# Optimization experiments

Hardware: AMD Instinct MI355X
Metric: run time of the kernel (lower is better)

The kernel has to match this reference:

```python
import jax, jax.numpy as jnp
import numpy as np

B, NPER, K = 32, 256, 32
N, E = B * NPER, B * NPER * 32
H, NF, NG, L = 128, 128, 50, 6
CUTOFF = 10.0
LOG2 = 0.6931471805599453


def _ssp(x):
    # ShiftedSoftplus: softplus(x) - log(2)
    return jax.nn.softplus(x) - LOG2


def setup_inputs() -> dict:
    key = jax.random.key(0)
    ks = jax.random.split(key, 16)
    rng = np.random.default_rng(0)

    pos = jnp.asarray(rng.uniform(0.0, 5.0, size=(N, 3)).astype(np.float32))
    z = jnp.asarray(rng.integers(1, 100, size=(N,)).astype(np.int32))
    batch = jnp.asarray((np.arange(N) // NPER).astype(np.int32))
    # K neighbors per atom, within the same graph, no self-loops; dst sorted
    dst = np.repeat(np.arange(N), K)
    off = rng.integers(1, NPER, size=N * K)
    src = (dst % NPER + off) % NPER + (dst // NPER) * NPER
    edge_index = jnp.asarray(np.stack([src, dst]).astype(np.int32))
    domain_ids = jnp.asarray(rng.integers(0, 5, size=(B,)).astype(np.int32))

    def dense(k, i, o):
        return jax.random.normal(k, (i, o), jnp.float32) / np.sqrt(i)

    def stackw(k, i, o):
        return jax.random.normal(k, (L, i, o), jnp.float32) / np.sqrt(i)

    return {
        'pos': pos, 'z': z, 'batch': batch, 'edge_index': edge_index,
        'domain_ids': domain_ids,
        'embedding': jax.random.normal(ks[0], (100, H), jnp.float32),
        'mlp_w1': stackw(ks[1], NG, NF), 'mlp_b1': jnp.zeros((L, NF), jnp.float32),
        'mlp_w2': stackw(ks[2], NF, NF), 'mlp_b2': jnp.zeros((L, NF), jnp.float32),
        'cf_lin1_w': stackw(ks[3], H, NF),
        'cf_lin2_w': stackw(ks[4], NF, H), 'cf_lin2_b': jnp.zeros((L, H), jnp.float32),
        'int_lin_w': stackw(ks[5], H, H), 'int_lin_b': jnp.zeros((L, H), jnp.float32),
        'out_w1': dense(ks[6], H, H // 2), 'out_b1': jnp.zeros((H // 2,), jnp.float32),
        'out_w2': dense(ks[7], H // 2, 1), 'out_b2': jnp.zeros((1,), jnp.float32),
        'dom_emb': jax.random.normal(ks[8], (5, 64), jnp.float32),
        'film_w1': dense(ks[9], 64, 128), 'film_b1': jnp.zeros((128,), jnp.float32),
        'film_w2': dense(ks[10], 128, 128), 'film_b2': jnp.zeros((128,), jnp.float32),
        'gamma_w': dense(ks[11], 128, H), 'gamma_b': jnp.zeros((H,), jnp.float32),
        'beta_w': dense(ks[12], 128, H), 'beta_b': jnp.zeros((H,), jnp.float32),
    }


def reference(pos, z, batch, edge_index, domain_ids, embedding,
              mlp_w1, mlp_b1, mlp_w2, mlp_b2, cf_lin1_w, cf_lin2_w, cf_lin2_b,
              int_lin_w, int_lin_b, out_w1, out_b1, out_w2, out_b2,
              dom_emb, film_w1, film_b1, film_w2, film_b2,
              gamma_w, gamma_b, beta_w, beta_b):
    n_atoms = pos.shape[0]
    n_graphs = domain_ids.shape[0]
    src, dst = edge_index[0], edge_index[1]

    # edge distances, gaussian smearing, cosine cutoff (computed once)
    d = jnp.sqrt(jnp.sum((pos[src] - pos[dst]) ** 2, axis=-1))          # [E]
    offsets = jnp.linspace(0.0, CUTOFF, NG).astype(pos.dtype)
    coeff = -0.5 / (CUTOFF / (NG - 1)) ** 2
    edge_attr = jnp.exp(coeff * (d[:, None] - offsets) ** 2)            # [E,NG]
    C = 0.5 * (jnp.cos(d * (np.pi / CUTOFF)) + 1.0)                     # [E]

    h = embedding[z]                                                    # [N,H]
    for l in range(L):
        # filter network on gaussian basis, modulated by cosine cutoff
        W = (_ssp(edge_attr @ mlp_w1[l] + mlp_b1[l]) @ mlp_w2[l] + mlp_b2[l]) * C[:, None]  # [E,NF]
        x = h @ cf_lin1_w[l]                                            # [N,NF]
        msg = x[src] * W                                                # [E,NF]
        agg = jax.ops.segment_sum(msg, dst, num_segments=n_atoms)       # [N,NF]
        x = agg @ cf_lin2_w[l] + cf_lin2_b[l]                           # [N,H]
        h = h + _ssp(x) @ int_lin_w[l] + int_lin_b[l]                   # residual

    atom_e = _ssp(h @ out_w1 + out_b1) @ out_w2 + out_b2                # [N,1]
    e_graph = jax.ops.segment_sum(atom_e, batch, num_segments=n_graphs) # [B,1]

    # FiLM domain bias (features are zeros, so gamma path contributes 0 - faithful)
    de = dom_emb[domain_ids]                                            # [B,64]
    film = jax.nn.relu(de @ film_w1 + film_b1) @ film_w2 + film_b2      # [B,128]
    gamma = film @ gamma_w + gamma_b                                    # [B,H]
    beta = film @ beta_w + beta_b                                       # [B,H]
    dummy = jnp.zeros((n_graphs, H), pos.dtype)
    bias = jnp.sum(gamma * dummy + beta, axis=-1)                       # [B]

    # faithful broadcast [B,1]+[B] -> [B,B], then sum(dim=1) as in original
    energy = jnp.sum(e_graph + bias[None, :], axis=1)                   # [B]

    forces = jnp.zeros((n_atoms, 3), energy.dtype)
    stress = jnp.zeros((n_graphs, 3, 3), energy.dtype)
    features = jnp.zeros((n_atoms, H), energy.dtype)
    return energy, forces, stress, features
```

## Files before the change

### kernel.cpp

```cpp
#include <hip/hip_runtime.h>
#include <math.h>

using uint = unsigned int;
typedef _Float16 h2    __attribute__((ext_vector_type(2)));
typedef _Float16 f16x8 __attribute__((ext_vector_type(8)));
typedef float    f32x4 __attribute__((ext_vector_type(4)));

#define N_ATOMS 8192
#define NEDGE   262144
#define KNBR    32
#define NGAUSS  50
#define NLAYER  6
#define NB      32
#define GTAB    2048
#define DMAX    8.6603f
#define FCUT    10.0f
#define MB      1048576

#define NSETUP  512

#define LSTRIDE 76
#define S_WT    0
#define S_AS    9728

#define WA_OFF  0
#define WB_OFF  8192
#define AS_OFF  16384
#define TS_OFF  17408
#define LAY_N   18432

#define T_W1    0
#define T_W2    4096
#define T_RBF   12288
#define T_HID   13312
#define TAB_SMEM 15360

#define OW1P_OFF 147456
#define PACK_END 151552
#define X_STR    524288

__device__ __forceinline__ float ssp(float x) {
    return fmaxf(x, 0.0f) + log1pf(expf(-fabsf(x))) - 0.69314718055994531f;
}
__device__ __forceinline__ uint pack2(float a, float b) {
    union { h2 h; uint u; } x;
    h2 v; v.x = (_Float16)a; v.y = (_Float16)b; x.h = v; return x.u;
}
__device__ __forceinline__ h2 u2h(uint u) {
    union { uint u; h2 h; } x; x.u = u; return x.h;
}
__device__ __forceinline__ uint h2u(h2 h) {
    union { h2 h; uint u; } x; x.h = h; return x.u;
}
__device__ __forceinline__ float fdot2f(h2 a, h2 b, float c) {
#if __has_builtin(__builtin_amdgcn_fdot2)
    return __builtin_amdgcn_fdot2(a, b, c, false);
#else
    return fmaf((float)a.y, (float)b.y, fmaf((float)a.x, (float)b.x, c));
#endif
}

__device__ __forceinline__ int swz(int row, int quad) {
    return row * 64 + ((quad ^ (row & 15)) << 2);
}
__device__ __forceinline__ int swzc(int row, int c) {
    return row * 64 + (((c >> 2) ^ (row & 15)) << 2) + (c & 3);
}

__device__ __forceinline__ void stage_sw(uint* dst, const uint* __restrict__ src,
                                         int n16, int tid) {
    for (int i = tid; i < n16; i += 256) {
        uint4 v = ((const uint4*)src)[i];
        *(uint4*)&dst[swz(i >> 4, i & 15)] = v;
    }
}

template<int NCT>
__device__ __forceinline__ void run_gemm_sw(const uint* smA, const uint* smW,
                                            int lane, int nb, f32x4* acc) {
    int m = lane & 15, q = lane >> 4;
    #pragma unroll
    for (int ks = 0; ks < 4; ++ks) {
        int cq = q + ks * 4;
        f16x8 a = *(const f16x8*)&smA[swz(m, cq)];
        #pragma unroll
        for (int ct = 0; ct < NCT; ++ct) {
            int n = nb + ct * 16 + m;
            f16x8 b = *(const f16x8*)&smW[swz(n, cq)];
            acc[ct] = __builtin_amdgcn_mfma_f32_16x16x32_f16(a, b, acc[ct], 0, 0, 0);
        }
    }
}

template<int NCT>
__device__ __forceinline__ void run_gemm(const uint* sm, int as_off, int lane,
                                         int nb, f32x4* acc) {
    int m = lane & 15, q = lane >> 4;
    #pragma unroll
    for (int ks = 0; ks < 4; ++ks) {
        f16x8 a = *(const f16x8*)&sm[as_off + m * LSTRIDE + q * 4 + ks * 16];
        #pragma unroll
        for (int ct = 0; ct < NCT; ++ct) {
            f16x8 b = *(const f16x8*)&sm[S_WT + (nb + ct * 16 + m) * LSTRIDE + q * 4 + ks * 16];
            acc[ct] = __builtin_amdgcn_mfma_f32_16x16x32_f16(a, b, acc[ct], 0, 0, 0);
        }
    }
}

struct SArgs {
    const float *pos; const int *z; const int *ei; const int *dom;
    const float *emb;
    const float *cf1; const float *cf2w; const float *intw; const float *ow1;
    const float *dome; const float *fw1; const float *fb1;
    const float *fw2; const float *fb2; const float *bw; const float *bb;
    uint *epack; float *h; uint *xA;
    float *gbias; uint *wpack; uint *bar;
    float *out; int out_size;
};

__global__ void __launch_bounds__(256) k_setup(SArgs a) {
    __shared__ __align__(16) uint sm[S_AS + 1216];
    const int tid = threadIdx.x, bid = blockIdx.x;
    const int gidx = bid * 256 + tid, gsz = NSETUP * 256;
    const int lane = tid & 63, w = tid >> 6;
    const int m = lane & 15, q = lane >> 4;
    const int rowbase = bid * 16;

    for (int i = gidx; i < a.out_size; i += gsz) a.out[i] = 0.0f;
    if (gidx < 256) a.bar[gidx] = 0u;

    for (int idx = gidx; idx < PACK_END; idx += gsz) {
        if (idx < OW1P_OFF) {
            int mat = idx >> 13, e = idx & 8191;
            int kp = e >> 7, cc = e & 127;
            const float* src = (mat < 6) ? (a.cf1 + mat * 16384)
                            : (mat < 12) ? (a.cf2w + (mat - 6) * 16384)
                                         : (a.intw + (mat - 12) * 16384);
            a.wpack[mat * 8192 + cc * 64 + kp] =
                pack2(src[2 * kp * 128 + cc], src[(2 * kp + 1) * 128 + cc]);
        } else {
            int e = idx - OW1P_OFF;
            int kp = e >> 6, cc = e & 63;
            a.wpack[OW1P_OFF + cc * 64 + kp] =
                pack2(a.ow1[2 * kp * 64 + cc], a.ow1[(2 * kp + 1) * 64 + cc]);
        }
    }

    const float invdelta = (float)(GTAB - 1) / DMAX;
    #pragma unroll
    for (int t = 0; t < 2; ++t) {
        int e = rowbase * KNBR + t * 256 + tid;
        int s = a.ei[e], d = a.ei[NEDGE + e];
        float dx = a.pos[3*s] - a.pos[3*d];
        float dy = a.pos[3*s+1] - a.pos[3*d+1];
        float dz = a.pos[3*s+2] - a.pos[3*d+2];
        float dist = sqrtf(dx*dx + dy*dy + dz*dz);
        float u = dist * invdelta;
        int i0 = (int)(u + 0.5f); i0 = (i0 < GTAB - 1) ? i0 : (GTAB - 1);
        a.epack[e] = (uint)s | ((uint)i0 << 16);
    }

    for (int i = tid; i < 1024; i += 256) {
        int r = i >> 6, f2 = i & 63;
        int zz = a.z[rowbase + r];
        float2 v = *(const float2*)&a.emb[zz * 128 + f2 * 2];
        *(float2*)&a.h[(rowbase + r) * 128 + f2 * 2] = v;
        sm[S_AS + r * LSTRIDE + f2] = pack2(v.x, v.y);
    }
    for (int i = tid; i < 2048; i += 256) {
        int m4 = i >> 7, cc = i & 127;
        float v[8];
        #pragma unroll
        for (int j = 0; j < 8; ++j) v[j] = a.cf1[(8 * m4 + j) * 128 + cc];
        uint4 pk; pk.x = pack2(v[0], v[1]); pk.y = pack2(v[2], v[3]);
        pk.z = pack2(v[4], v[5]); pk.w = pack2(v[6], v[7]);
        *(uint4*)&sm[cc * LSTRIDE + m4 * 4] = pk;
    }
    __syncthreads();
    {
        f32x4 acc[2] = {{0,0,0,0},{0,0,0,0}};
        run_gemm<2>(sm, S_AS, lane, w * 32, acc);
        #pragma unroll
        for (int ct = 0; ct < 2; ++ct) {
            int n = w * 32 + ct * 16 + m;
            #pragma unroll
            for (int i = 0; i < 4; ++i) {
                float v = acc[ct][i];
                float u = __shfl_xor(v, 1, 64);
                if (!(lane & 1))
                    a.xA[(rowbase + q * 4 + i) * 64 + (n >> 1)] = pack2(v, u);
            }
        }
    }
    __syncthreads();
    if (bid >= 32 && bid < 64) {
        int g = bid - 32;
        float* fs = (float*)sm;
        if (tid < 64) fs[tid] = a.dome[a.dom[g] * 64 + tid];
        __syncthreads();
        if (tid < 128) {
            float acc = a.fb1[tid];
            for (int i = 0; i < 64; ++i) acc = fmaf(fs[i], a.fw1[i*128 + tid], acc);
            fs[64 + tid] = fmaxf(acc, 0.0f);
        }
        __syncthreads();
        if (tid < 128) {
            float acc = a.fb2[tid];
            for (int i = 0; i < 128; ++i) acc = fmaf(fs[64+i], a.fw2[i*128 + tid], acc);
            fs[192 + tid] = acc;
        }
        __syncthreads();
        if (tid < 128) {
            float acc = a.bb[tid];
            for (int i = 0; i < 128; ++i) acc = fmaf(fs[192+i], a.bw[i*128 + tid], acc);
            #pragma unroll
            for (int off = 32; off > 0; off >>= 1) acc += __shfl_down(acc, off, 64);
            if ((tid & 63) == 0) fs[320 + (tid >> 6)] = acc;
        }
        __syncthreads();
        if (tid == 0) a.gbias[g] = fs[320] + fs[321];
    }
}

__global__ void __launch_bounds__(256) k_table(
    const float* __restrict__ mw1, const float* __restrict__ mb1,
    const float* __restrict__ mw2, const float* __restrict__ mb2,
    uint* __restrict__ tab) {
    __shared__ __align__(16) uint sm[TAB_SMEM];
    const int tid = threadIdx.x;
    const int l = blockIdx.x >> 6;
    const int base = (blockIdx.x & 63) * 32;
    for (int i = tid; i < 4096; i += 256) {
        int kp = i >> 7, cc = i & 127, g0 = 2 * kp;
        float va = (g0 < NGAUSS)     ? mw1[l*NGAUSS*128 + g0*128 + cc]     : 0.f;
        float vb = (g0 + 1 < NGAUSS) ? mw1[l*NGAUSS*128 + (g0+1)*128 + cc] : 0.f;
        sm[T_W1 + i] = pack2(va, vb);
    }
    for (int i = tid; i < 8192; i += 256) {
        int kp = i >> 7, cc = i & 127;
        sm[T_W2 + i] = pack2(mw2[l*16384 + 2*kp*128 + cc],
                             mw2[l*16384 + (2*kp+1)*128 + cc]);
    }
    const float delta = DMAX / (float)(GTAB - 1);
    const float gstep = FCUT / (float)(NGAUSS - 1);
    const float coeff = -0.5f / (gstep * gstep);
    for (int i = tid; i < 1024; i += 256) {
        int r = i >> 5, kp = i & 31;
        float dv = (float)(base + r) * delta;
        int g0 = 2 * kp;
        float v0 = 0.f, v1 = 0.f;
        if (g0 < NGAUSS)     { float t = dv - (float)g0 * gstep;     v0 = expf(coeff*t*t); }
        if (g0 + 1 < NGAUSS) { float t = dv - (float)(g0+1) * gstep; v1 = expf(coeff*t*t); }
        sm[T_RBF + i] = pack2(v0, v1);
    }
    __syncthreads();
    int tx = tid & 31, ty = tid >> 5, c0 = tx * 4, tr0 = ty * 4;
    float acc[4][4];
    #pragma unroll
    for (int i = 0; i < 4; ++i) { acc[i][0]=0.f; acc[i][1]=0.f; acc[i][2]=0.f; acc[i][3]=0.f; }
    #pragma unroll
    for (int oct = 0; oct < 8; ++oct) {
        int kp0 = oct * 4;
        uint4 w_[4];
        #pragma unroll
        for (int p = 0; p < 4; ++p) w_[p] = *(const uint4*)&sm[T_W1 + (kp0+p)*128 + c0];
        #pragma unroll
        for (int i = 0; i < 4; ++i) {
            uint4 av = *(const uint4*)&sm[T_RBF + (tr0+i)*32 + kp0];
            uint aa[4] = {av.x, av.y, av.z, av.w};
            #pragma unroll
            for (int p = 0; p < 4; ++p) {
                h2 ap = u2h(aa[p]);
                acc[i][0] = fdot2f(ap, u2h(w_[p].x), acc[i][0]);
                acc[i][1] = fdot2f(ap, u2h(w_[p].y), acc[i][1]);
                acc[i][2] = fdot2f(ap, u2h(w_[p].z), acc[i][2]);
                acc[i][3] = fdot2f(ap, u2h(w_[p].w), acc[i][3]);
            }
        }
    }
    float4 b1v = *(const float4*)&mb1[l*128 + c0];
    #pragma unroll
    for (int i = 0; i < 4; ++i) {
        uint2 o;
        o.x = pack2(ssp(acc[i][0] + b1v.x), ssp(acc[i][1] + b1v.y));
        o.y = pack2(ssp(acc[i][2] + b1v.z), ssp(acc[i][3] + b1v.w));
        *(uint2*)&sm[T_HID + (tr0+i)*64 + (c0 >> 1)] = o;
    }
    __syncthreads();
    float acc2[4][4];
    #pragma unroll
    for (int i = 0; i < 4; ++i) { acc2[i][0]=0.f; acc2[i][1]=0.f; acc2[i][2]=0.f; acc2[i][3]=0.f; }
    #pragma unroll 4
    for (int oct = 0; oct < 16; ++oct) {
        int kp0 = oct * 4;
        uint4 w_[4];
        #pragma unroll
        for (int p = 0; p < 4; ++p) w_[p] = *(const uint4*)&sm[T_W2 + (kp0+p)*128 + c0];
        #pragma unroll
        for (int i = 0; i < 4; ++i) {
            uint4 av = *(const uint4*)&sm[T_HID + (tr0+i)*64 + kp0];
            uint aa[4] = {av.x, av.y, av.z, av.w};
            #pragma unroll
            for (int p = 0; p < 4; ++p) {
                h2 ap = u2h(aa[p]);
                acc2[i][0] = fdot2f(ap, u2h(w_[p].x), acc2[i][0]);
                acc2[i][1] = fdot2f(ap, u2h(w_[p].y), acc2[i][1]);
                acc2[i][2] = fdot2f(ap, u2h(w_[p].z), acc2[i][2]);
                acc2[i][3] = fdot2f(ap, u2h(w_[p].w), acc2[i][3]);
            }
        }
    }
    float4 b2v = *(const float4*)&mb2[l*128 + c0];
    #pragma unroll
    for (int i = 0; i < 4; ++i) {
        int row = base + tr0 + i;
        float dv = (float)row * delta;
        float Cd = 0.5f * (cosf(dv * 0.3141592653589793f) + 1.0f);
        uint2 o;
        o.x = pack2((acc2[i][0] + b2v.x)*Cd, (acc2[i][1] + b2v.y)*Cd);
        o.y = pack2((acc2[i][2] + b2v.z)*Cd, (acc2[i][3] + b2v.w)*Cd);
        *(uint2*)&tab[(l*GTAB + row)*64 + tx*2] = o;
    }
}

struct LArgs {
    const float* h;
    const uint* x0;
    uint* xb;
    const uint* tab;
    const uint* epack;
    const uint* wpack;
    const float* cf2b;
    const float* intb;
    const float* ob1; const float* ow2; const float* ob2;
    const float* gbias;
    float* out;
    uint* bar;
};

__global__ void __launch_bounds__(256, 2) k_fused(LArgs a) {
    __shared__ __align__(16) uint sm[LAY_N];
    const int tid = threadIdx.x, bid = blockIdx.x;
    const int lane = tid & 63, w = tid >> 6;
    const int m = lane & 15, q = lane >> 4;
    const int xcd = bid & 7;
    const int j   = bid >> 3;
    const int g   = xcd * 4 + (j >> 4);
    const int sub = j & 15;
    const int rowbase = g * 256 + sub * 16;

    float hr[2][4];
    #pragma unroll
    for (int ct = 0; ct < 2; ++ct)
        #pragma unroll
        for (int i = 0; i < 4; ++i)
            hr[ct][i] = a.h[(rowbase + q * 4 + i) * 128 + w * 32 + ct * 16 + m];

    const uint* xr = a.x0;
    uint* xw = a.xb;

    #pragma unroll 1
    for (int l = 0; l < NLAYER; ++l) {
        const bool last = (l == NLAYER - 1);
        const uint* w2p  = a.wpack + (6 + l) * 8192;
        const uint* w3p  = a.wpack + (12 + l) * 8192;
        const uint* w1np = last ? (a.wpack + OW1P_OFF) : (a.wpack + (l + 1) * 8192);
        const uint* tabl = a.tab + l * (GTAB * 64);
        const float* b2 = a.cf2b + l * 128;
        const float* b3 = a.intb + l * 128;

        stage_sw(&sm[WA_OFF], w2p, 2048, tid);
        {
            const int side = lane >> 5, l5 = lane & 31;
            #pragma unroll
            for (int p = 0; p < 4; ++p) {
                int al = p * 4 + w;
                uint ep = a.epack[(rowbase + al) * KNBR + l5];
                h2 a0; a0.x = (_Float16)0; a0.y = (_Float16)0;
                h2 a1 = a0;
                #pragma unroll 4
                for (int k = 0; k < 16; ++k) {
                    uint v = __shfl(ep, 2 * k + side, 64);
                    uint2 tv = *(const uint2*)&tabl[(v >> 16) * 64 + l5 * 2];
                    uint2 xv = *(const uint2*)&xr[(v & 0xffffu) * 64 + l5 * 2];
                    a0 = a0 + u2h(xv.x) * u2h(tv.x);
                    a1 = a1 + u2h(xv.y) * u2h(tv.y);
                }
                uint u0 = h2u(a0), u1 = h2u(a1);
                uint p0 = __shfl_xor(u0, 32, 64), p1 = __shfl_xor(u1, 32, 64);
                if (side == 0) {
                    h2 r0 = u2h(u0) + u2h(p0), r1 = u2h(u1) + u2h(p1);
                    uint2 o; o.x = h2u(r0); o.y = h2u(r1);
                    *(uint2*)&sm[AS_OFF + swzc(al, l5 * 2)] = o;
                }
            }
        }
        __syncthreads();
        stage_sw(&sm[WB_OFF], w3p, 2048, tid);
        {
            f32x4 acc[2] = {{0,0,0,0},{0,0,0,0}};
            run_gemm_sw<2>(&sm[AS_OFF], &sm[WA_OFF], lane, w * 32, acc);
            #pragma unroll
            for (int ct = 0; ct < 2; ++ct) {
                int n = w * 32 + ct * 16 + m;
                float bv = b2[n];
                #pragma unroll
                for (int i = 0; i < 4; ++i) {
                    float v = ssp(acc[ct][i] + bv);
                    float u = __shfl_xor(v, 1, 64);
                    if (!(lane & 1))
                        sm[TS_OFF + swzc(q * 4 + i, n >> 1)] = pack2(v, u);
                }
            }
        }
        __syncthreads();
        stage_sw(&sm[WA_OFF], w1np, last ? 1024 : 2048, tid);
        {
            f32x4 acc[2] = {{0,0,0,0},{0,0,0,0}};
            run_gemm_sw<2>(&sm[TS_OFF], &sm[WB_OFF], lane, w * 32, acc);
            #pragma unroll
            for (int ct = 0; ct < 2; ++ct) {
                int n = w * 32 + ct * 16 + m;
                float bv = b3[n];
                #pragma unroll
                for (int i = 0; i < 4; ++i) {
                    float hv = hr[ct][i] + acc[ct][i] + bv;
                    hr[ct][i] = hv;
                    float u = __shfl_xor(hv, 1, 64);
                    if (!(lane & 1))
                        sm[AS_OFF + swzc(q * 4 + i, n >> 1)] = pack2(hv, u);
                }
            }
        }
        __syncthreads();
        if (!last) {
            f32x4 acc[2] = {{0,0,0,0},{0,0,0,0}};
            run_gemm_sw<2>(&sm[AS_OFF], &sm[WA_OFF], lane, w * 32, acc);
            #pragma unroll
            for (int ct = 0; ct < 2; ++ct) {
                int n = w * 32 + ct * 16 + m;
                #pragma unroll
                for (int i = 0; i < 4; ++i) {
                    float v = acc[ct][i];
                    float u = __shfl_xor(v, 1, 64);
                    if (!(lane & 1))
                        xw[(rowbase + q * 4 + i) * 64 + (n >> 1)] = pack2(v, u);
                }
            }
            __syncthreads();
            if (tid == 0) {
                uint* c = a.bar + l * NB + g;
                __hip_atomic_fetch_add(c, 1u, __ATOMIC_RELAXED,
                                       __HIP_MEMORY_SCOPE_AGENT);
                int it = 0;
                while (__hip_atomic_load(c, __ATOMIC_RELAXED,
                                         __HIP_MEMORY_SCOPE_AGENT) < 16u
                       && ++it < (1 << 19))
                    __builtin_amdgcn_s_sleep(1);
            }
            __syncthreads();
            xr = xw; xw += X_STR;
        } else {
            f32x4 acc[1] = {{0,0,0,0}};
            run_gemm_sw<1>(&sm[AS_OFF], &sm[WA_OFF], lane, w * 16, acc);
            int n = w * 16 + m;
            float b1v = a.ob1[n], w2v = a.ow2[n];
            float part = 0.f;
            #pragma unroll
            for (int i = 0; i < 4; ++i) part += ssp(acc[0][i] + b1v) * w2v;
            #pragma unroll
            for (int mm = 1; mm < 64; mm <<= 1) part += __shfl_xor(part, mm, 64);
            float* fs = (float*)&sm[TS_OFF];
            if (lane == 0) fs[w] = part;
            __syncthreads();
            if (tid == 0) {
                float bsum = fs[0] + fs[1] + fs[2] + fs[3] + 16.0f * a.ob2[0];
                float add = 32.0f * bsum;
                if (sub == 0) {
                    float sb = 0.f;
                    for (int jj = 0; jj < NB; ++jj) sb += a.gbias[jj];
                    add += sb;
                }
                atomicAdd(&a.out[g], add);
            }
        }
    }
}

extern "C" void kernel_launch(void* const* d_in, const int* in_sizes, int n_in,
                              void* d_out, int out_size, void* d_ws, size_t ws_size,
                              hipStream_t stream) {
    SArgs a;
    a.pos  = (const float*)d_in[0];
    a.z    = (const int*)d_in[1];
    a.ei   = (const int*)d_in[3];
    a.dom  = (const int*)d_in[4];
    a.emb  = (const float*)d_in[5];
    const float* mw1 = (const float*)d_in[6];
    const float* mb1 = (const float*)d_in[7];
    const float* mw2 = (const float*)d_in[8];
    const float* mb2 = (const float*)d_in[9];
    a.cf1  = (const float*)d_in[10];
    a.cf2w = (const float*)d_in[11];
    const float* cf2b = (const float*)d_in[12];
    a.intw = (const float*)d_in[13];
    const float* intb = (const float*)d_in[14];
    a.ow1  = (const float*)d_in[15];
    const float* ob1  = (const float*)d_in[16];
    const float* ow2  = (const float*)d_in[17];
    const float* ob2  = (const float*)d_in[18];
    a.dome = (const float*)d_in[19];
    a.fw1  = (const float*)d_in[20];
    a.fb1  = (const float*)d_in[21];
    a.fw2  = (const float*)d_in[22];
    a.fb2  = (const float*)d_in[23];
    a.bw   = (const float*)d_in[26];
    a.bb   = (const float*)d_in[27];

    char* ws = (char*)d_ws;
    a.epack   = (uint*)(ws + 0);
    uint* tab = (uint*)(ws + 2*MB);
    a.h       = (float*)(ws + 5*MB);
    a.xA      = (uint*)(ws + 9*MB);
    uint* xb  = (uint*)(ws + 11*MB);
    a.gbias   = (float*)(ws + 21*MB);
    a.bar     = (uint*)(ws + 21*MB + 4096);
    a.wpack   = (uint*)(ws + 21*MB + 8192);
    a.out = (float*)d_out;
    a.out_size = out_size;

    k_setup<<<NSETUP, 256, 0, stream>>>(a);
    k_table<<<384, 256, 0, stream>>>(mw1, mb1, mw2, mb2, tab);

    LArgs la;
    la.h = a.h; la.x0 = a.xA; la.xb = xb;
    la.tab = tab; la.epack = a.epack; la.wpack = a.wpack;
    la.cf2b = cf2b; la.intb = intb;
    la.ob1 = ob1; la.ow2 = ow2; la.ob2 = ob2;
    la.gbias = a.gbias; la.out = (float*)d_out; la.bar = a.bar;

    k_fused<<<dim3(512), dim3(256), 0, stream>>>(la);
}
```

Before: 275.6 us.

## Replace persistent fused kernel with per-layer launches instead of spin barriers

The single persistent kernel, which synchronized 16 blocks per graph through atomic spin-wait counters between layers, is split into six per-layer kernel launches that use kernel boundaries as the barrier. The hidden state h is now written to global memory each layer and reloaded at the next launch instead of staying in registers, and x is ping-ponged between two buffers. This removes the spin-wait overhead and the occupancy hint of 2 blocks, at the cost of extra launch overhead and an extra global round trip for h on every layer.

Result: no change. 273.6 us (-0.7%).

```diff
diff --git a/kernel.cpp b/kernel.cpp
--- a/kernel.cpp
+++ b/kernel.cpp
@@ -37,7 +37,6 @@
 
 #define OW1P_OFF 147456
 #define PACK_END 151552
-#define X_STR    524288
 
 __device__ __forceinline__ float ssp(float x) {
     return fmaxf(x, 0.0f) + log1pf(expf(-fabsf(x))) - 0.69314718055994531f;
@@ -114,7 +113,7 @@
     const float *dome; const float *fw1; const float *fb1;
     const float *fw2; const float *fb2; const float *bw; const float *bb;
     uint *epack; float *h; uint *xA;
-    float *gbias; uint *wpack; uint *bar;
+    float *gbias; uint *wpack;
     float *out; int out_size;
 };
 
@@ -127,7 +126,6 @@
     const int rowbase = bid * 16;
 
     for (int i = gidx; i < a.out_size; i += gsz) a.out[i] = 0.0f;
-    if (gidx < 256) a.bar[gidx] = 0u;
 
     for (int idx = gidx; idx < PACK_END; idx += gsz) {
         if (idx < OW1P_OFF) {
@@ -323,22 +321,16 @@
     }
 }
 
-struct LArgs {
-    const float* h;
-    const uint* x0;
-    uint* xb;
-    const uint* tab;
-    const uint* epack;
-    const uint* wpack;
-    const float* cf2b;
-    const float* intb;
-    const float* ob1; const float* ow2; const float* ob2;
-    const float* gbias;
-    float* out;
-    uint* bar;
-};
-
-__global__ void __launch_bounds__(256, 2) k_fused(LArgs a) {
+template<bool LAST>
+__global__ void __launch_bounds__(256) k_layer(
+    float* __restrict__ h, const uint* __restrict__ xin, uint* __restrict__ xout,
+    const uint* __restrict__ tabl, const uint* __restrict__ epack,
+    const uint* __restrict__ w2p, const uint* __restrict__ w3p,
+    const uint* __restrict__ w1np,
+    const float* __restrict__ b2, const float* __restrict__ b3,
+    const float* __restrict__ ob1, const float* __restrict__ ow2,
+    const float* __restrict__ ob2, const float* __restrict__ gbias,
+    float* __restrict__ out) {
     __shared__ __align__(16) uint sm[LAY_N];
     const int tid = threadIdx.x, bid = blockIdx.x;
     const int lane = tid & 63, w = tid >> 6;
@@ -354,135 +346,109 @@
     for (int ct = 0; ct < 2; ++ct)
         #pragma unroll
         for (int i = 0; i < 4; ++i)
-            hr[ct][i] = a.h[(rowbase + q * 4 + i) * 128 + w * 32 + ct * 16 + m];
-
-    const uint* xr = a.x0;
-    uint* xw = a.xb;
-
-    #pragma unroll 1
-    for (int l = 0; l < NLAYER; ++l) {
-        const bool last = (l == NLAYER - 1);
-        const uint* w2p  = a.wpack + (6 + l) * 8192;
-        const uint* w3p  = a.wpack + (12 + l) * 8192;
-        const uint* w1np = last ? (a.wpack + OW1P_OFF) : (a.wpack + (l + 1) * 8192);
-        const uint* tabl = a.tab + l * (GTAB * 64);
-        const float* b2 = a.cf2b + l * 128;
-        const float* b3 = a.intb + l * 128;
-
-        stage_sw(&sm[WA_OFF], w2p, 2048, tid);
-        {
-            const int side = lane >> 5, l5 = lane & 31;
-            #pragma unroll
-            for (int p = 0; p < 4; ++p) {
-                int al = p * 4 + w;
-                uint ep = a.epack[(rowbase + al) * KNBR + l5];
-                h2 a0; a0.x = (_Float16)0; a0.y = (_Float16)0;
-                h2 a1 = a0;
-                #pragma unroll 4
-                for (int k = 0; k < 16; ++k) {
-                    uint v = __shfl(ep, 2 * k + side, 64);
-                    uint2 tv = *(const uint2*)&tabl[(v >> 16) * 64 + l5 * 2];
-                    uint2 xv = *(const uint2*)&xr[(v & 0xffffu) * 64 + l5 * 2];
-                    a0 = a0 + u2h(xv.x) * u2h(tv.x);
-                    a1 = a1 + u2h(xv.y) * u2h(tv.y);
-                }
-                uint u0 = h2u(a0), u1 = h2u(a1);
-                uint p0 = __shfl_xor(u0, 32, 64), p1 = __shfl_xor(u1, 32, 64);
-                if (side == 0) {
-                    h2 r0 = u2h(u0) + u2h(p0), r1 = u2h(u1) + u2h(p1);
-                    uint2 o; o.x = h2u(r0); o.y = h2u(r1);
-                    *(uint2*)&sm[AS_OFF + swzc(al, l5 * 2)] = o;
-                }
-            }
-        }
+            hr[ct][i] = h[(rowbase + q * 4 + i) * 128 + w * 32 + ct * 16 + m];
+
+    stage_sw(&sm[WA_OFF], w2p, 2048, tid);
+    {
+        const int side = lane >> 5, l5 = lane & 31;
+        #pragma unroll
+        for (int p = 0; p < 4; ++p) {
+            int al = p * 4 + w;
+            uint ep = epack[(rowbase + al) * KNBR + l5];
+            h2 a0; a0.x = (_Float16)0; a0.y = (_Float16)0;
+            h2 a1 = a0;
+            #pragma unroll 4
+            for (int k = 0; k < 16; ++k) {
+                uint v = __shfl(ep, 2 * k + side, 64);
+                uint2 tv = *(const uint2*)&tabl[(v >> 16) * 64 + l5 * 2];
+                uint2 xv = *(const uint2*)&xin[(v & 0xffffu) * 64 + l5 * 2];
+                a0 = a0 + u2h(xv.x) * u2h(tv.x);
+                a1 = a1 + u2h(xv.y) * u2h(tv.y);
+            }
+            uint u0 = h2u(a0), u1 = h2u(a1);
+            uint p0 = __shfl_xor(u0, 32, 64), p1 = __shfl_xor(u1, 32, 64);
+            if (side == 0) {
+                h2 r0 = u2h(u0) + u2h(p0), r1 = u2h(u1) + u2h(p1);
+                uint2 o; o.x = h2u(r0); o.y = h2u(r1);
+                *(uint2*)&sm[AS_OFF + swzc(al, l5 * 2)] = o;
+            }
+        }
+    }
+    __syncthreads();
+    stage_sw(&sm[WB_OFF], w3p, 2048, tid);
+    {
+        f32x4 acc[2] = {{0,0,0,0},{0,0,0,0}};
+        run_gemm_sw<2>(&sm[AS_OFF], &sm[WA_OFF], lane, w * 32, acc);
+        #pragma unroll
+        for (int ct = 0; ct < 2; ++ct) {
+            int n = w * 32 + ct * 16 + m;
+            float bv = b2[n];
+            #pragma unroll
+            for (int i = 0; i < 4; ++i) {
+                float v = ssp(acc[ct][i] + bv);
+                float u = __shfl_xor(v, 1, 64);
+                if (!(lane & 1))
+                    sm[TS_OFF + swzc(q * 4 + i, n >> 1)] = pack2(v, u);
+            }
+        }
+    }
+    __syncthreads();
+    stage_sw(&sm[WA_OFF], w1np, LAST ? 1024 : 2048, tid);
+    {
+        f32x4 acc[2] = {{0,0,0,0},{0,0,0,0}};
+        run_gemm_sw<2>(&sm[TS_OFF], &sm[WB_OFF], lane, w * 32, acc);
+        #pragma unroll
+        for (int ct = 0; ct < 2; ++ct) {
+            int n = w * 32 + ct * 16 + m;
+            float bv = b3[n];
+            #pragma unroll
+            for (int i = 0; i < 4; ++i) {
+                int r = rowbase + q * 4 + i;
+                float hv = hr[ct][i] + acc[ct][i] + bv;
+                h[r * 128 + n] = hv;
+                float u = __shfl_xor(hv, 1, 64);
+                if (!(lane & 1))
+                    sm[AS_OFF + swzc(q * 4 + i, n >> 1)] = pack2(hv, u);
+            }
+        }
+    }
+    __syncthreads();
+    if (!LAST) {
+        f32x4 acc[2] = {{0,0,0,0},{0,0,0,0}};
+        run_gemm_sw<2>(&sm[AS_OFF], &sm[WA_OFF], lane, w * 32, acc);
+        #pragma unroll
+        for (int ct = 0; ct < 2; ++ct) {
+            int n = w * 32 + ct * 16 + m;
+            #pragma unroll
+            for (int i = 0; i < 4; ++i) {
+                float v = acc[ct][i];
+                float u = __shfl_xor(v, 1, 64);
+                if (!(lane & 1))
+                    xout[(rowbase + q * 4 + i) * 64 + (n >> 1)] = pack2(v, u);
+            }
+        }
+    } else {
+        f32x4 acc[1] = {{0,0,0,0}};
+        run_gemm_sw<1>(&sm[AS_OFF], &sm[WA_OFF], lane, w * 16, acc);
+        int n = w * 16 + m;
+        float b1v = ob1[n], w2v = ow2[n];
+        float part = 0.f;
+        #pragma unroll
+        for (int i = 0; i < 4; ++i) part += ssp(acc[0][i] + b1v) * w2v;
+        #pragma unroll
+        for (int mm = 1; mm < 64; mm <<= 1) part += __shfl_xor(part, mm, 64);
+        float* fs = (float*)&sm[TS_OFF];
+        if (lane == 0) fs[w] = part;
         __syncthreads();
-        stage_sw(&sm[WB_OFF], w3p, 2048, tid);
-        {
-            f32x4 acc[2] = {{0,0,0,0},{0,0,0,0}};
-            run_gemm_sw<2>(&sm[AS_OFF], &sm[WA_OFF], lane, w * 32, acc);
-            #pragma unroll
-            for (int ct = 0; ct < 2; ++ct) {
-                int n = w * 32 + ct * 16 + m;
-                float bv = b2[n];
-                #pragma unroll
-                for (int i = 0; i < 4; ++i) {
-                    float v = ssp(acc[ct][i] + bv);
-                    float u = __shfl_xor(v, 1, 64);
-                    if (!(lane & 1))
-                        sm[TS_OFF + swzc(q * 4 + i, n >> 1)] = pack2(v, u);
-                }
-            }
-        }
-        __syncthreads();
-        stage_sw(&sm[WA_OFF], w1np, last ? 1024 : 2048, tid);
-        {
-            f32x4 acc[2] = {{0,0,0,0},{0,0,0,0}};
-            run_gemm_sw<2>(&sm[TS_OFF], &sm[WB_OFF], lane, w * 32, acc);
-            #pragma unroll
-            for (int ct = 0; ct < 2; ++ct) {
-                int n = w * 32 + ct * 16 + m;
-                float bv = b3[n];
-                #pragma unroll
-                for (int i = 0; i < 4; ++i) {
-                    float hv = hr[ct][i] + acc[ct][i] + bv;
-                    hr[ct][i] = hv;
-                    float u = __shfl_xor(hv, 1, 64);
-                    if (!(lane & 1))
-                        sm[AS_OFF + swzc(q * 4 + i, n >> 1)] = pack2(hv, u);
-                }
-            }
-        }
-        __syncthreads();
-        if (!last) {
-            f32x4 acc[2] = {{0,0,0,0},{0,0,0,0}};
-            run_gemm_sw<2>(&sm[AS_OFF], &sm[WA_OFF], lane, w * 32, acc);
-            #pragma unroll
-            for (int ct = 0; ct < 2; ++ct) {
-                int n = w * 32 + ct * 16 + m;
-                #pragma unroll
-                for (int i = 0; i < 4; ++i) {
-                    float v = acc[ct][i];
-                    float u = __shfl_xor(v, 1, 64);
-                    if (!(lane & 1))
-                        xw[(rowbase + q * 4 + i) * 64 + (n >> 1)] = pack2(v, u);
-                }
-            }
-            __syncthreads();
-            if (tid == 0) {
-                uint* c = a.bar + l * NB + g;
-                __hip_atomic_fetch_add(c, 1u, __ATOMIC_RELAXED,
-                                       __HIP_MEMORY_SCOPE_AGENT);
-                int it = 0;
-                while (__hip_atomic_load(c, __ATOMIC_RELAXED,
-                                         __HIP_MEMORY_SCOPE_AGENT) < 16u
-                       && ++it < (1 << 19))
-                    __builtin_amdgcn_s_sleep(1);
-            }
-            __syncthreads();
-            xr = xw; xw += X_STR;
-        } else {
-            f32x4 acc[1] = {{0,0,0,0}};
-            run_gemm_sw<1>(&sm[AS_OFF], &sm[WA_OFF], lane, w * 16, acc);
-            int n = w * 16 + m;
-            float b1v = a.ob1[n], w2v = a.ow2[n];
-            float part = 0.f;
-            #pragma unroll
-            for (int i = 0; i < 4; ++i) part += ssp(acc[0][i] + b1v) * w2v;
-            #pragma unroll
-            for (int mm = 1; mm < 64; mm <<= 1) part += __shfl_xor(part, mm, 64);
-            float* fs = (float*)&sm[TS_OFF];
-            if (lane == 0) fs[w] = part;
-            __syncthreads();
-            if (tid == 0) {
-                float bsum = fs[0] + fs[1] + fs[2] + fs[3] + 16.0f * a.ob2[0];
-                float add = 32.0f * bsum;
-                if (sub == 0) {
-                    float sb = 0.f;
-                    for (int jj = 0; jj < NB; ++jj) sb += a.gbias[jj];
-                    add += sb;
-                }
-                atomicAdd(&a.out[g], add);
-            }
+        if (tid == 0) {
+            float bsum = fs[0] + fs[1] + fs[2] + fs[3] + 16.0f * ob2[0];
+            float add = 32.0f * bsum;
+            if (sub == 0) {
+                float sb = 0.f;
+                for (int jj = 0; jj < NB; ++jj) sb += gbias[jj];
+                add += sb;
+            }
+            atomicAdd(&out[g], add);
         }
     }
 }
@@ -522,22 +488,31 @@
     uint* tab = (uint*)(ws + 2*MB);
     a.h       = (float*)(ws + 5*MB);
     a.xA      = (uint*)(ws + 9*MB);
-    uint* xb  = (uint*)(ws + 11*MB);
-    a.gbias   = (float*)(ws + 21*MB);
-    a.bar     = (uint*)(ws + 21*MB + 4096);
-    a.wpack   = (uint*)(ws + 21*MB + 8192);
+    uint* xB  = (uint*)(ws + 11*MB);
+    a.gbias   = (float*)(ws + 15*MB);
+    a.wpack   = (uint*)(ws + 15*MB + 4096);
     a.out = (float*)d_out;
     a.out_size = out_size;
 
     k_setup<<<NSETUP, 256, 0, stream>>>(a);
     k_table<<<384, 256, 0, stream>>>(mw1, mb1, mw2, mb2, tab);
 
-    LArgs la;
-    la.h = a.h; la.x0 = a.xA; la.xb = xb;
-    la.tab = tab; la.epack = a.epack; la.wpack = a.wpack;
-    la.cf2b = cf2b; la.intb = intb;
-    la.ob1 = ob1; la.ow2 = ow2; la.ob2 = ob2;
-    la.gbias = a.gbias; la.out = (float*)d_out; la.bar = a.bar;
-
-    k_fused<<<dim3(512), dim3(256), 0, stream>>>(la);
-}
+    const uint* xr = a.xA;
+    uint* xw = xB;
+    for (int l = 0; l < NLAYER; ++l) {
+        const uint* w2p = a.wpack + (6 + l) * 8192;
+        const uint* w3p = a.wpack + (12 + l) * 8192;
+        if (l < NLAYER - 1) {
+            k_layer<false><<<512, 256, 0, stream>>>(
+                a.h, xr, xw, tab + l*GTAB*64, a.epack, w2p, w3p,
+                a.wpack + (l + 1) * 8192,
+                cf2b + l*128, intb + l*128, ob1, ow2, ob2, a.gbias, a.out);
+        } else {
+            k_layer<true><<<512, 256, 0, stream>>>(
+                a.h, xr, xw, tab + l*GTAB*64, a.epack, w2p, w3p,
+                a.wpack + OW1P_OFF,
+                cf2b + l*128, intb + l*128, ob1, ow2, ob2, a.gbias, a.out);
+        }
+        const uint* tmp = xr; xr = xw; xw = (uint*)tmp;
+    }
+}
```
